# Performance work log

Measured on AMD Instinct MI355X. Metric: run time of the kernel, lower is better.

## Reference

```python
import jax, jax.numpy as jnp
import numpy as np

B, S, D_MODEL = 1, 1024, 1024
D_CKV, D_CQ = 256, 512
N_HEAD, D_HEAD, D_ROPE = 8, 64, 32


def setup_inputs() -> dict:
    key = jax.random.key(0)
    ks = jax.random.split(key, 12)
    def w(k, shape):
        return jax.random.normal(k, shape, dtype=jnp.float32) * 0.02
    return {
        "x": jax.random.normal(ks[0], (B, S, D_MODEL), dtype=jnp.float32),
        "w_q_idx": w(ks[1], (D_MODEL, N_HEAD * D_HEAD)),
        "w_k_idx": w(ks[2], (D_MODEL, D_HEAD)),
        "w_idx": jnp.ones((N_HEAD,), dtype=jnp.float32),
        "raw_delta": jnp.zeros((D_ROPE // 2,), dtype=jnp.float32),
        "w_dkv": w(ks[3], (D_MODEL, D_CKV)),
        "w_uk": w(ks[4], (D_CKV, N_HEAD * D_HEAD)),
        "w_uv": w(ks[5], (D_CKV, N_HEAD * D_HEAD)),
        "w_dq": w(ks[6], (D_MODEL, D_CQ)),
        "w_uq": w(ks[7], (D_CQ, N_HEAD * D_HEAD)),
        "w_qr": w(ks[8], (D_CQ, N_HEAD * D_ROPE)),
        "w_kr": w(ks[9], (D_MODEL, D_ROPE)),
        "w_out": w(ks[10], (N_HEAD * D_HEAD, D_MODEL)),
        "k_ts": 128,
        "local_window": 64,
    }


def _pope(x, raw_delta, theta):
    # x: (b, L, H, d_rope); positions run along axis 1 (matches torch PoPE)
    delta = -2.0 * jnp.pi * jax.nn.sigmoid(raw_delta)            # (d2,)
    pos = jnp.arange(x.shape[1], dtype=x.dtype)
    ang = pos[None, :, None, None] * theta + delta               # (1, L, 1, d2)
    c, s = jnp.cos(ang), jnp.sin(ang)
    mu1, mu2 = jnp.split(jax.nn.softplus(x), 2, axis=-1)
    return jnp.concatenate((mu1 * c - mu2 * s, mu1 * s + mu2 * c), axis=-1)


def reference(x, w_q_idx, w_k_idx, w_idx, raw_delta, w_dkv, w_uk, w_uv,
              w_dq, w_uq, w_qr, w_kr, w_out, k_ts, local_window):
    b, s, _ = x.shape
    h, dh, dr = N_HEAD, D_HEAD, D_ROPE
    theta = 1.0 / (10000.0 ** (2.0 * jnp.arange(dr // 2, dtype=jnp.float32) / dr))

    # ---- LightningIndexer: per-head relu'd relevance, combined with learned head weights
    qI = (x @ w_q_idx).reshape(b, s, h, dh)
    kI = x @ w_k_idx                                             # (b, s, dh)
    sc = jax.nn.relu(jnp.einsum('bthd,bsd->bths', qI, kI))
    I = jnp.einsum('bths,h->bts', sc, w_idx)

    # ---- TokenSelector: force local window in, mask future out, top-k indices
    qp = jnp.arange(s)[:, None]
    kp = jnp.arange(s)[None, :]
    local = (kp >= qp - local_window + 1) & (kp <= qp)
    causal = kp > qp
    I = jnp.where(local, jnp.inf, I)
    I = jnp.where(causal, -jnp.inf, I)
    k = min(k_ts, s)
    _, idx = jax.lax.top_k(I, k)                                 # (b, s, k) int32

    gather = jax.vmap(lambda t, i: t[i])                         # (s,d),(l,k)->(l,k,d)

    # ---- MLA latent KV, gathered per query
    c_kv = x @ w_dkv                                             # (b, s, d_ckv)
    ckv_sel = gather(c_kv, idx)                                  # (b, s, k, d_ckv)
    key_c = (ckv_sel @ w_uk).reshape(b, s, k, h, dh).transpose(0, 3, 1, 2, 4)
    value = (ckv_sel @ w_uv).reshape(b, s, k, h, dh).transpose(0, 3, 1, 2, 4)

    c_q = x @ w_dq
    query_c = (c_q @ w_uq).reshape(b, s, h, dh).transpose(0, 2, 1, 3)
    query_r = _pope((c_q @ w_qr).reshape(b, s, h, dr), raw_delta, theta).transpose(0, 2, 1, 3)

    # key rope: PoPE applied with positions along the k (selected-token) axis,
    # exactly as the torch code's permute(0,2,1,3) does
    x_sel = gather(x, idx)                                       # (b, s, k, d_model)
    kr = _pope((x_sel @ w_kr).transpose(0, 2, 1, 3), raw_delta, theta).transpose(0, 2, 1, 3)
    key_r = jnp.broadcast_to(kr[:, None], (b, h, s, k, dr))

    query = jnp.concatenate((query_c, query_r), axis=-1)         # (b, h, s, dh+dr)
    keyt = jnp.concatenate((key_c, key_r), axis=-1)              # (b, h, s, k, dh+dr)
    scale = (dh + dr) ** -0.5
    scores = jnp.einsum('bhld,bhlkd->bhlk', query, keyt) * scale
    attn = jax.nn.softmax(scores, axis=-1)
    out = jnp.einsum('bhlk,bhlkd->bhld', attn, value)
    out = out.transpose(0, 2, 1, 3).reshape(b, s, h * dh)
    return out @ w_out
```

## Files before the change

### kernel.cpp

```cpp
#include <hip/hip_runtime.h>
#include <math.h>

#define S_LEN 1024
#define NH 8

typedef __attribute__((ext_vector_type(8))) short bf16x8;
typedef __attribute__((ext_vector_type(4))) float f32x4;

__device__ __forceinline__ float sp_softplus(float x) {
    return fmaxf(x, 0.f) + log1pf(expf(-fabsf(x)));
}

__device__ __forceinline__ unsigned short bfu(float f) {
    unsigned u = __float_as_uint(f);
    unsigned r = (u + 0x7FFFu + ((u >> 16) & 1u)) >> 16;
    return (unsigned short)r;
}

struct FRONT {
    const float *x, *wqidx, *wkidx, *raw_delta, *wuk;
    const float *wdkv, *wdq, *wkr, *wuq, *wqr, *wuv, *wout;
    float *qIP, *kIP, *csc, *css;
    unsigned short *wdkvT, *wdqT, *wkrT, *wuqT, *wqrT, *wuvT, *woutT, *wukb;
};

__global__ __launch_bounds__(256) void front_kernel(FRONT f)
{
    __shared__ float As[2][16][18];
    __shared__ float Bs[2][16][68];
    __shared__ unsigned short tile[64][65];
    int bx = blockIdx.x;
    if (bx < 1152) {
        int gx = bx % 18, gy = bx / 18;
        int half = threadIdx.x >> 7;
        int t = threadIdx.x & 127;
        int u = gx * 2 + half;
        const float* B; float* C;
        int ldb, N, n0, kb;
        if (u < 32) {
            B = f.wqidx; ldb = 512; N = 512;
            C = f.qIP + (long)(u >> 3) * 524288;
            n0 = (u & 7) * 64;
            kb = (u >> 3) * 256;
        } else {
            B = f.wkidx; ldb = 64; N = 64;
            C = f.kIP + (long)(u - 32) * 65536;
            n0 = 0;
            kb = (u - 32) * 256;
        }
        int ke = kb + 256;
        int m0 = gy * 16;
        int ar = t >> 2, ak = t & 3;
        int bk = t >> 3, bn = t & 7;
        int ty = t >> 4, tx = t & 15;

        float4 aN = make_float4(0.f, 0.f, 0.f, 0.f);
        if (t < 64) aN = *(const float4*)(f.x + (long)(m0 + ar) * 1024 + kb + ak * 4);
        float4 b0 = *(const float4*)(B + (long)(kb + bk) * ldb + n0 + bn * 4);
        float4 b1 = *(const float4*)(B + (long)(kb + bk) * ldb + n0 + (bn + 8) * 4);
        float acc[2][4] = {};
        for (int k0 = kb; k0 < ke; k0 += 16) {
            if (t < 64) {
                As[half][ak * 4 + 0][ar] = aN.x;
                As[half][ak * 4 + 1][ar] = aN.y;
                As[half][ak * 4 + 2][ar] = aN.z;
                As[half][ak * 4 + 3][ar] = aN.w;
            }
            *(float4*)&Bs[half][bk][bn * 4] = b0;
            *(float4*)&Bs[half][bk][(bn + 8) * 4] = b1;
            __syncthreads();
            if (k0 + 16 < ke) {
                if (t < 64) aN = *(const float4*)(f.x + (long)(m0 + ar) * 1024 + (k0 + 16) + ak * 4);
                b0 = *(const float4*)(B + (long)(k0 + 16 + bk) * ldb + n0 + bn * 4);
                b1 = *(const float4*)(B + (long)(k0 + 16 + bk) * ldb + n0 + (bn + 8) * 4);
            }
            #pragma unroll
            for (int kk = 0; kk < 16; ++kk) {
                float2 a = *(float2*)&As[half][kk][ty * 2];
                float4 b = *(float4*)&Bs[half][kk][tx * 4];
                acc[0][0] += a.x * b.x; acc[0][1] += a.x * b.y;
                acc[0][2] += a.x * b.z; acc[0][3] += a.x * b.w;
                acc[1][0] += a.y * b.x; acc[1][1] += a.y * b.y;
                acc[1][2] += a.y * b.z; acc[1][3] += a.y * b.w;
            }
            __syncthreads();
        }
        #pragma unroll
        for (int i = 0; i < 2; ++i) {
            float4 v = make_float4(acc[i][0], acc[i][1], acc[i][2], acc[i][3]);
            *(float4*)(C + (long)(m0 + ty * 2 + i) * N + n0 + tx * 4) = v;
        }
    } else if (bx < 1616) {
        int b = bx - 1152;
        const float* srcs[7] = {f.wdkv, f.wdq, f.wkr, f.wuq, f.wqr, f.wuv, f.wout};
        unsigned short* dsts[7] = {f.wdkvT, f.wdqT, f.wkrT, f.wuqT, f.wqrT, f.wuvT, f.woutT};
        const int Ns[7]   = {256, 512, 32, 512, 256, 512, 1024};
        const int Klds[7] = {1024, 1024, 1024, 512, 512, 256, 512};
        const int Ntl[7]  = {4, 8, 1, 8, 4, 8, 16};
        const int bst[8]  = {0, 64, 192, 208, 272, 304, 336, 464};
        int e = 0;
        #pragma unroll
        for (int i = 1; i < 7; ++i) if (b >= bst[i]) e = i;
        int lb = b - bst[e];
        int nt = lb % Ntl[e], kt = lb / Ntl[e];
        const float* src = srcs[e];
        unsigned short* dst = dsts[e];
        int N = Ns[e], Kld = Klds[e];
        int k0 = kt * 64, n0 = nt * 64;
        int t = threadIdx.x;
        int c = t & 63, r4 = t >> 6;
        #pragma unroll
        for (int it = 0; it < 16; ++it) {
            int r = it * 4 + r4;
            float v = (n0 + c < N) ? src[(long)(k0 + r) * N + n0 + c] : 0.f;
            tile[r][c] = bfu(v);
        }
        __syncthreads();
        int wq = t & 7;
        #pragma unroll
        for (int itw = 0; itw < 2; ++itw) {
            int wr = itw * 32 + (t >> 3);
            if (n0 + wr < N) {
                unsigned short v[8];
                #pragma unroll
                for (int j = 0; j < 8; ++j) v[j] = tile[wq * 8 + j][wr];
                *(uint4*)(dst + (long)(n0 + wr) * Kld + k0 + wq * 8) = *(uint4*)v;
            }
        }
    } else if (bx < 1624) {
        int idx = (bx - 1616) * 256 + threadIdx.x;
        int j = idx >> 4, i = idx & 15;
        float rd = f.raw_delta[i];
        float delta = -6.283185307179586f * (1.f / (1.f + expf(-rd)));
        float th = exp2f(-(float)i * 0.83048202372184f);
        float ang = (float)j * th + delta;
        float sv, cv;
        sincosf(ang, &sv, &cv);
        f.csc[idx] = cv;
        f.css[idx] = sv;
    } else {
        int idx = (bx - 1624) * 256 + threadIdx.x;
        f.wukb[idx] = bfu(f.wuk[idx]);
    }
}

struct MFG {
    const float* A[10]; const unsigned short* B[10]; float* C[10];
    int lda[10], ldb[10], ldc[10], K[10], N[10], obf[10];
    int tstart[11]; int ne;
};

__global__ __launch_bounds__(256) void mgemm(MFG mg)
{
    int bx = blockIdx.x, e = 0;
    #pragma unroll
    for (int i = 1; i < 10; ++i) if (i < mg.ne && bx >= mg.tstart[i]) e = i;
    const float* A = mg.A[e];
    const unsigned short* B = mg.B[e];
    float* C = mg.C[e];
    int lda = mg.lda[e], ldb = mg.ldb[e], ldc = mg.ldc[e];
    int K = mg.K[e], N = mg.N[e];
    int m0 = blockIdx.y * 64, n0 = (bx - mg.tstart[e]) * 64;

    __shared__ unsigned short As[64][40];
    __shared__ unsigned short Bs[64][40];
    int t = threadIdx.x;
    int srow = t >> 2, skq = t & 3;
    int wid = t >> 6, l = t & 63;
    int wm = (wid >> 1) * 32, wn = (wid & 1) * 32;
    int fr = l & 15, fk = (l >> 4) * 8;
    bool bok = (n0 + srow) < N;

    f32x4 acc00 = {0.f, 0.f, 0.f, 0.f};
    f32x4 acc01 = {0.f, 0.f, 0.f, 0.f};
    f32x4 acc10 = {0.f, 0.f, 0.f, 0.f};
    f32x4 acc11 = {0.f, 0.f, 0.f, 0.f};

    for (int k0 = 0; k0 < K; k0 += 32) {
        {
            const float* ap = A + (long)(m0 + srow) * lda + k0 + skq * 8;
            float4 v0 = *(const float4*)ap;
            float4 v1 = *(const float4*)(ap + 4);
            unsigned short* d = &As[srow][skq * 8];
            d[0] = bfu(v0.x); d[1] = bfu(v0.y); d[2] = bfu(v0.z); d[3] = bfu(v0.w);
            d[4] = bfu(v1.x); d[5] = bfu(v1.y); d[6] = bfu(v1.z); d[7] = bfu(v1.w);
        }
        {
            uint4 bv = make_uint4(0u, 0u, 0u, 0u);
            if (bok) bv = *(const uint4*)(B + (long)(n0 + srow) * ldb + k0 + skq * 8);
            *(uint4*)&Bs[srow][skq * 8] = bv;
        }
        __syncthreads();
        bf16x8 a0 = *(bf16x8*)&As[wm + fr][fk];
        bf16x8 a1 = *(bf16x8*)&As[wm + 16 + fr][fk];
        bf16x8 b0 = *(bf16x8*)&Bs[wn + fr][fk];
        bf16x8 b1 = *(bf16x8*)&Bs[wn + 16 + fr][fk];
        acc00 = __builtin_amdgcn_mfma_f32_16x16x32_bf16(a0, b0, acc00, 0, 0, 0);
        acc01 = __builtin_amdgcn_mfma_f32_16x16x32_bf16(a0, b1, acc01, 0, 0, 0);
        acc10 = __builtin_amdgcn_mfma_f32_16x16x32_bf16(a1, b0, acc10, 0, 0, 0);
        acc11 = __builtin_amdgcn_mfma_f32_16x16x32_bf16(a1, b1, acc11, 0, 0, 0);
        __syncthreads();
    }
    int crow = (l >> 4) * 4;
    int col0 = n0 + wn + fr, col1 = n0 + wn + 16 + fr;
    if (mg.obf[e]) {
        unsigned short* Cu = (unsigned short*)C;
        if (col0 < N) {
            #pragma unroll
            for (int r = 0; r < 4; ++r) {
                Cu[(long)(m0 + wm + crow + r) * ldc + col0]      = bfu(acc00[r]);
                Cu[(long)(m0 + wm + 16 + crow + r) * ldc + col0] = bfu(acc10[r]);
            }
        }
        if (col1 < N) {
            #pragma unroll
            for (int r = 0; r < 4; ++r) {
                Cu[(long)(m0 + wm + crow + r) * ldc + col1]      = bfu(acc01[r]);
                Cu[(long)(m0 + wm + 16 + crow + r) * ldc + col1] = bfu(acc11[r]);
            }
        }
    } else {
        if (col0 < N) {
            #pragma unroll
            for (int r = 0; r < 4; ++r) {
                C[(long)(m0 + wm + crow + r) * ldc + col0]      = acc00[r];
                C[(long)(m0 + wm + 16 + crow + r) * ldc + col0] = acc10[r];
            }
        }
        if (col1 < N) {
            #pragma unroll
            for (int r = 0; r < 4; ++r) {
                C[(long)(m0 + wm + crow + r) * ldc + col1]      = acc01[r];
                C[(long)(m0 + wm + 16 + crow + r) * ldc + col1] = acc11[r];
            }
        }
    }
}

struct MIDARG {
    const float *qIP, *kIP, *w_idx; float* I;
    const float* qc; const unsigned short* wukb; float* qabs;
    const float *qrp, *raw_delta; float* qrr;
    const float* xkr; float* mu;
};

__global__ __launch_bounds__(256) void mid_kernel(MIDARG g)
{
    __shared__ __align__(16) char smem[26112];
    int b = blockIdx.x;
    int t = threadIdx.x;
    if (b < 512) {
        int sb = b % 16, tb = b / 16;
        if (sb * 64 > tb * 32 + 31) return;
        int t0 = tb * 32, s0 = sb * 64;
        float (*ksT)[68] = (float(*)[68])smem;
        float (*qs)[68]  = (float(*)[68])(smem + 17408);
        {
            int r = t & 63, q = t >> 6;
            #pragma unroll
            for (int u = 0; u < 4; ++u) {
                int c4 = q * 4 + u;
                long off = (long)(s0 + r) * 64 + c4 * 4;
                float4 v = *(const float4*)(g.kIP + off);
                #pragma unroll
                for (int s = 1; s < 4; ++s) {
                    float4 v2 = *(const float4*)(g.kIP + (long)s * 65536 + off);
                    v.x += v2.x; v.y += v2.y; v.z += v2.z; v.w += v2.w;
                }
                ksT[c4 * 4 + 0][r] = v.x;
                ksT[c4 * 4 + 1][r] = v.y;
                ksT[c4 * 4 + 2][r] = v.z;
                ksT[c4 * 4 + 3][r] = v.w;
            }
        }
        int ty = t >> 4, tx = t & 15;
        float accI[2][4] = {};
        for (int h = 0; h < 8; ++h) {
            __syncthreads();
            {
                int r = t >> 3, q = t & 7;
                long base = (long)(t0 + r) * 512 + h * 64;
                #pragma unroll
                for (int half = 0; half < 2; ++half) {
                    long off = base + (q + half * 8) * 4;
                    float4 a = *(const float4*)(g.qIP + off);
                    #pragma unroll
                    for (int s = 1; s < 4; ++s) {
                        float4 a1 = *(const float4*)(g.qIP + (long)s * 524288 + off);
                        a.x += a1.x; a.y += a1.y; a.z += a1.z; a.w += a1.w;
                    }
                    *(float4*)&qs[r][(q + half * 8) * 4] = a;
                }
            }
            __syncthreads();
            float acc[2][4] = {};
            #pragma unroll
            for (int dc = 0; dc < 4; ++dc) {
                float a0[16], a1[16];
                #pragma unroll
                for (int u = 0; u < 4; ++u) {
                    float4 v0 = *(float4*)&qs[ty * 2][dc * 16 + u * 4];
                    float4 v1 = *(float4*)&qs[ty * 2 + 1][dc * 16 + u * 4];
                    a0[u * 4 + 0] = v0.x; a0[u * 4 + 1] = v0.y; a0[u * 4 + 2] = v0.z; a0[u * 4 + 3] = v0.w;
                    a1[u * 4 + 0] = v1.x; a1[u * 4 + 1] = v1.y; a1[u * 4 + 2] = v1.z; a1[u * 4 + 3] = v1.w;
                }
                #pragma unroll
                for (int kk = 0; kk < 16; ++kk) {
                    int d = dc * 16 + kk;
                    float4 bb = *(float4*)&ksT[d][tx * 4];
                    acc[0][0] += a0[kk] * bb.x; acc[0][1] += a0[kk] * bb.y;
                    acc[0][2] += a0[kk] * bb.z; acc[0][3] += a0[kk] * bb.w;
                    acc[1][0] += a1[kk] * bb.x; acc[1][1] += a1[kk] * bb.y;
                    acc[1][2] += a1[kk] * bb.z; acc[1][3] += a1[kk] * bb.w;
                }
            }
            float wh = g.w_idx[h];
            #pragma unroll
            for (int i = 0; i < 2; ++i)
                #pragma unroll
                for (int j = 0; j < 4; ++j)
                    accI[i][j] += wh * fmaxf(acc[i][j], 0.f);
        }
        #pragma unroll
        for (int i = 0; i < 2; ++i) {
            float4 v = make_float4(accI[i][0], accI[i][1], accI[i][2], accI[i][3]);
            *(float4*)&g.I[(long)(t0 + ty * 2 + i) * 1024 + s0 + tx * 4] = v;
        }
    } else if (b < 1024) {
        int lb = b - 512;
        int h = lb >> 6, rem = lb & 63;
        int n0 = (rem >> 4) * 64, m0 = (rem & 15) * 64;
        const float* A = g.qc + h * 64;
        const unsigned short* B = g.wukb + h * 64;
        float* C = g.qabs + h * 256;
        unsigned short (*As)[40] = (unsigned short(*)[40])smem;
        unsigned short (*Bs)[40] = (unsigned short(*)[40])(smem + 5120);
        int srow = t >> 2, skq = t & 3;
        int wid = t >> 6, l = t & 63;
        int wm = (wid >> 1) * 32, wn = (wid & 1) * 32;
        int fr = l & 15, fk = (l >> 4) * 8;
        f32x4 acc00 = {0.f, 0.f, 0.f, 0.f};
        f32x4 acc01 = {0.f, 0.f, 0.f, 0.f};
        f32x4 acc10 = {0.f, 0.f, 0.f, 0.f};
        f32x4 acc11 = {0.f, 0.f, 0.f, 0.f};
        for (int k0 = 0; k0 < 64; k0 += 32) {
            {
                const float* ap = A + (long)(m0 + srow) * 512 + k0 + skq * 8;
                float4 v0 = *(const float4*)ap;
                float4 v1 = *(const float4*)(ap + 4);
                unsigned short* d = &As[srow][skq * 8];
                d[0] = bfu(v0.x); d[1] = bfu(v0.y); d[2] = bfu(v0.z); d[3] = bfu(v0.w);
                d[4] = bfu(v1.x); d[5] = bfu(v1.y); d[6] = bfu(v1.z); d[7] = bfu(v1.w);
            }
            {
                uint4 bv = *(const uint4*)(B + (long)(n0 + srow) * 512 + k0 + skq * 8);
                *(uint4*)&Bs[srow][skq * 8] = bv;
            }
            __syncthreads();
            bf16x8 a0 = *(bf16x8*)&As[wm + fr][fk];
            bf16x8 a1 = *(bf16x8*)&As[wm + 16 + fr][fk];
            bf16x8 b0 = *(bf16x8*)&Bs[wn + fr][fk];
            bf16x8 b1 = *(bf16x8*)&Bs[wn + 16 + fr][fk];
            acc00 = __builtin_amdgcn_mfma_f32_16x16x32_bf16(a0, b0, acc00, 0, 0, 0);
            acc01 = __builtin_amdgcn_mfma_f32_16x16x32_bf16(a0, b1, acc01, 0, 0, 0);
            acc10 = __builtin_amdgcn_mfma_f32_16x16x32_bf16(a1, b0, acc10, 0, 0, 0);
            acc11 = __builtin_amdgcn_mfma_f32_16x16x32_bf16(a1, b1, acc11, 0, 0, 0);
            __syncthreads();
        }
        int crow = (l >> 4) * 4;
        int col0 = n0 + wn + fr, col1 = n0 + wn + 16 + fr;
        #pragma unroll
        for (int r = 0; r < 4; ++r) {
            C[(long)(m0 + wm + crow + r) * 2048 + col0]      = acc00[r];
            C[(long)(m0 + wm + 16 + crow + r) * 2048 + col0] = acc10[r];
            C[(long)(m0 + wm + crow + r) * 2048 + col1]      = acc01[r];
            C[(long)(m0 + wm + 16 + crow + r) * 2048 + col1] = acc11[r];
        }
    } else if (b < 1536) {
        int tq = (b - 1024) * 2 + (t >> 7);
        int tt = t & 127;
        int h = tt >> 4, i = tt & 15;
        float rd = g.raw_delta[i];
        float delta = -6.283185307179586f * (1.f / (1.f + expf(-rd)));
        float th = exp2f(-(float)i * 0.83048202372184f);
        float ang = (float)tq * th + delta;
        float sv, cv;
        sincosf(ang, &sv, &cv);
        float m1 = sp_softplus(g.qrp[tq * 256 + h * 32 + i]);
        float m2 = sp_softplus(g.qrp[tq * 256 + h * 32 + 16 + i]);
        g.qrr[tq * 256 + h * 32 + i]      = m1 * cv - m2 * sv;
        g.qrr[tq * 256 + h * 32 + 16 + i] = m1 * sv + m2 * cv;
    } else {
        int i = (b - 1536) * 256 + t;
        g.mu[i] = sp_softplus(g.xkr[i]);
    }
}

__global__ __launch_bounds__(256) void topk_kernel(
    const float* __restrict__ I, int* __restrict__ idxout)
{
    int t = blockIdx.x * 4 + (threadIdx.x >> 6);
    int lane = threadIdx.x & 63;
    int smin = max(0, t - 63);
    int w = min(64, t + 1);
    if (lane < w) idxout[t * 128 + lane] = smin + lane;
    for (int q = t + 1 + lane; q < 128; q += 64)
        idxout[t * 128 + q] = q;
    int f = max(0, t - 63);
    int m = min(f, 64);
    if (m == 0) return;
    const float* row = I + (long)t * 1024;

    unsigned long long key[16];
    #pragma unroll
    for (int g4 = 0; g4 < 4; ++g4) {
        float4 v = *(const float4*)(row + lane * 16 + g4 * 4);
        float vv[4] = {v.x, v.y, v.z, v.w};
        #pragma unroll
        for (int j = 0; j < 4; ++j) {
            int s = lane * 16 + g4 * 4 + j;
            unsigned long long k = 0ull;
            if (s < f) {
                unsigned u = __float_as_uint(vv[j]);
                unsigned ou = (u & 0x80000000u) ? ~u : (u | 0x80000000u);
                k = ((unsigned long long)ou << 32) | (0xFFFFFFFFu - (unsigned)s);
            }
            key[g4 * 4 + j] = k;
        }
    }

    #pragma unroll
    for (int km = 1; km <= 10; ++km) {
        #pragma unroll
        for (int jm = km - 1; jm >= 0; --jm) {
            if (jm >= 4) {
                int lmask = 1 << (jm - 4);
                #pragma unroll
                for (int r = 0; r < 16; ++r) {
                    unsigned long long other = __shfl_xor(key[r], lmask, 64);
                    int i = lane * 16 + r;
                    bool keep_max = (((i & (1 << km)) == 0) == ((i & (1 << jm)) == 0));
                    unsigned long long mx = key[r] > other ? key[r] : other;
                    unsigned long long mn = key[r] > other ? other : key[r];
                    key[r] = keep_max ? mx : mn;
                }
            } else {
                int rmask = 1 << jm;
                #pragma unroll
                for (int r = 0; r < 16; ++r) {
                    if ((r & rmask) == 0) {
                        int r2 = r | rmask;
                        int i = lane * 16 + r;
                        bool keep_max_low = ((i & (1 << km)) == 0);
                        unsigned long long a = key[r], b = key[r2];
                        unsigned long long mx = a > b ? a : b;
                        unsigned long long mn = a > b ? b : a;
                        key[r]  = keep_max_low ? mx : mn;
                        key[r2] = keep_max_low ? mn : mx;
                    }
                }
            }
        }
    }

    if (lane < 4) {
        #pragma unroll
        for (int r = 0; r < 16; ++r) {
            int e = lane * 16 + r;
            if (e < m) {
                int s = (int)(0xFFFFFFFFu - (unsigned)(key[r] & 0xFFFFFFFFull));
                idxout[t * 128 + w + e] = s;
            }
        }
    }
}

__global__ __launch_bounds__(256) void attn_kernel(
    const float* __restrict__ qabs, const float* __restrict__ qrr,
    const unsigned short* __restrict__ ckvb, const float* __restrict__ mu,
    const float* __restrict__ csc, const float* __restrict__ css,
    const int* __restrict__ idxb, float* __restrict__ olat)
{
    __shared__ float sc[8][68];
    __shared__ float hs[16];
    __shared__ int idx_s[128];

    int t = blockIdx.x, tid = threadIdx.x;
    int w = tid >> 6, l = tid & 63;
    const float scale = 0.10206207261596575f;

    if (tid < 128) idx_s[tid] = idxb[t * 128 + tid];

    int hrow = l & 15;
    int kslice = (l >> 4) * 8;
    int hpv = l >> 3;
    int c8 = w * 64 + (l & 7) * 8;

    float mrun0 = -INFINITY, mrun1 = -INFINITY;
    float lrun0 = 0.f, lrun1 = 0.f;
    float acc0 = 0, acc1 = 0, acc2 = 0, acc3 = 0;
    float acc4 = 0, acc5 = 0, acc6 = 0, acc7 = 0;

    __syncthreads();

    #pragma unroll
    for (int chunk = 0; chunk < 2; ++chunk) {
        if (chunk) __syncthreads();

        int r = w * 16 + hrow;
        int src = idx_s[chunk * 64 + r];
        int jglob = chunk * 64 + r;
        f32x4 st = {0.f, 0.f, 0.f, 0.f};
        #pragma unroll 1
        for (int ks = 0; ks < 8; ++ks) {
            bf16x8 af = *(const bf16x8*)(ckvb + (long)src * 256 + ks * 32 + kslice);
            bf16x8 qf = {0, 0, 0, 0, 0, 0, 0, 0};
            if (hrow < 8) {
                const float* qp = qabs + (long)t * 2048 + hrow * 256 + ks * 32 + kslice;
                float4 a = *(const float4*)qp;
                float4 b = *(const float4*)(qp + 4);
                unsigned short qq[8];
                qq[0] = bfu(a.x * scale); qq[1] = bfu(a.y * scale);
                qq[2] = bfu(a.z * scale); qq[3] = bfu(a.w * scale);
                qq[4] = bfu(b.x * scale); qq[5] = bfu(b.y * scale);
                qq[6] = bfu(b.z * scale); qq[7] = bfu(b.w * scale);
                qf = *(bf16x8*)qq;
            }
            st = __builtin_amdgcn_mfma_f32_16x16x32_bf16(af, qf, st, 0, 0, 0);
        }
        {
            int i15 = kslice & 15;
            bool lo = kslice < 16;
            float4 m1a = *(const float4*)(mu + src * 32 + i15);
            float4 m1b = *(const float4*)(mu + src * 32 + i15 + 4);
            float4 m2a = *(const float4*)(mu + src * 32 + 16 + i15);
            float4 m2b = *(const float4*)(mu + src * 32 + 16 + i15 + 4);
            float4 ca = *(const float4*)(csc + jglob * 16 + i15);
            float4 cb = *(const float4*)(csc + jglob * 16 + i15 + 4);
            float4 sa = *(const float4*)(css + jglob * 16 + i15);
            float4 sb = *(const float4*)(css + jglob * 16 + i15 + 4);
            unsigned short hh[8];
            hh[0] = bfu(lo ? m1a.x * ca.x - m2a.x * sa.x : m1a.x * sa.x + m2a.x * ca.x);
            hh[1] = bfu(lo ? m1a.y * ca.y - m2a.y * sa.y : m1a.y * sa.y + m2a.y * ca.y);
            hh[2] = bfu(lo ? m1a.z * ca.z - m2a.z * sa.z : m1a.z * sa.z + m2a.z * ca.z);
            hh[3] = bfu(lo ? m1a.w * ca.w - m2a.w * sa.w : m1a.w * sa.w + m2a.w * ca.w);
            hh[4] = bfu(lo ? m1b.x * cb.x - m2b.x * sb.x : m1b.x * sb.x + m2b.x * cb.x);
            hh[5] = bfu(lo ? m1b.y * cb.y - m2b.y * sb.y : m1b.y * sb.y + m2b.y * cb.y);
            hh[6] = bfu(lo ? m1b.z * cb.z - m2b.z * sb.z : m1b.z * sb.z + m2b.z * cb.z);
            hh[7] = bfu(lo ? m1b.w * cb.w - m2b.w * sb.w : m1b.w * sb.w + m2b.w * cb.w);
            bf16x8 af = *(bf16x8*)hh;
            bf16x8 qf = {0, 0, 0, 0, 0, 0, 0, 0};
            if (hrow < 8) {
                const float* qp = qrr + (long)t * 256 + hrow * 32 + kslice;
                float4 a = *(const float4*)qp;
                float4 b = *(const float4*)(qp + 4);
                unsigned short qq[8];
                qq[0] = bfu(a.x * scale); qq[1] = bfu(a.y * scale);
                qq[2] = bfu(a.z * scale); qq[3] = bfu(a.w * scale);
                qq[4] = bfu(b.x * scale); qq[5] = bfu(b.y * scale);
                qq[6] = bfu(b.z * scale); qq[7] = bfu(b.w * scale);
                qf = *(bf16x8*)qq;
            }
            st = __builtin_amdgcn_mfma_f32_16x16x32_bf16(af, qf, st, 0, 0, 0);
        }
        {
            int srow2 = w * 16 + (l >> 4) * 4;
            if (hrow < 8) {
                #pragma unroll
                for (int rr = 0; rr < 4; ++rr) sc[hrow][srow2 + rr] = st[rr];
            }
        }
        __syncthreads();

        float rh0, rh1;
        {
            int h = 2 * w;
            float v = sc[h][l];
            float mx = v;
            #pragma unroll
            for (int off = 32; off > 0; off >>= 1) mx = fmaxf(mx, __shfl_xor(mx, off));
            float mnew = fmaxf(mrun0, mx);
            float p = expf(v - mnew);
            float ps = p;
            #pragma unroll
            for (int off = 32; off > 0; off >>= 1) ps += __shfl_xor(ps, off);
            rh0 = expf(mrun0 - mnew);
            lrun0 = lrun0 * rh0 + ps;
            mrun0 = mnew;
            sc[h][l] = p;
        }
        {
            int h = 2 * w + 1;
            float v = sc[h][l];
            float mx = v;
            #pragma unroll
            for (int off = 32; off > 0; off >>= 1) mx = fmaxf(mx, __shfl_xor(mx, off));
            float mnew = fmaxf(mrun1, mx);
            float p = expf(v - mnew);
            float ps = p;
            #pragma unroll
            for (int off = 32; off > 0; off >>= 1) ps += __shfl_xor(ps, off);
            rh1 = expf(mrun1 - mnew);
            lrun1 = lrun1 * rh1 + ps;
            mrun1 = mnew;
            sc[h][l] = p;
        }
        if (l == 0) {
            hs[2 * w] = rh0;
            hs[2 * w + 1] = rh1;
            if (chunk == 1) {
                hs[8 + 2 * w] = lrun0;
                hs[8 + 2 * w + 1] = lrun1;
            }
        }
        __syncthreads();

        float rsel = hs[hpv];
        acc0 *= rsel; acc1 *= rsel; acc2 *= rsel; acc3 *= rsel;
        acc4 *= rsel; acc5 *= rsel; acc6 *= rsel; acc7 *= rsel;
        #pragma unroll 4
        for (int j = 0; j < 64; ++j) {
            float p = sc[hpv][j];
            int srcj = idx_s[chunk * 64 + j];
            uint4 vv = *(const uint4*)(ckvb + (long)srcj * 256 + c8);
            acc0 += p * __uint_as_float(vv.x << 16);
            acc1 += p * __uint_as_float(vv.x & 0xffff0000u);
            acc2 += p * __uint_as_float(vv.y << 16);
            acc3 += p * __uint_as_float(vv.y & 0xffff0000u);
            acc4 += p * __uint_as_float(vv.z << 16);
            acc5 += p * __uint_as_float(vv.z & 0xffff0000u);
            acc6 += p * __uint_as_float(vv.w << 16);
            acc7 += p * __uint_as_float(vv.w & 0xffff0000u);
        }
    }

    float inv = 1.f / hs[8 + hpv];
    float* op = olat + (long)t * 2048 + hpv * 256 + c8;
    *(float4*)op       = make_float4(acc0 * inv, acc1 * inv, acc2 * inv, acc3 * inv);
    *(float4*)(op + 4) = make_float4(acc4 * inv, acc5 * inv, acc6 * inv, acc7 * inv);
}

extern "C" void kernel_launch(void* const* d_in, const int* in_sizes, int n_in,
                              void* d_out, int out_size, void* d_ws, size_t ws_size,
                              hipStream_t stream)
{
    const float* x         = (const float*)d_in[0];
    const float* w_q_idx   = (const float*)d_in[1];
    const float* w_k_idx   = (const float*)d_in[2];
    const float* w_idx     = (const float*)d_in[3];
    const float* raw_delta = (const float*)d_in[4];
    const float* w_dkv     = (const float*)d_in[5];
    const float* w_uk      = (const float*)d_in[6];
    const float* w_uv      = (const float*)d_in[7];
    const float* w_dq      = (const float*)d_in[8];
    const float* w_uq      = (const float*)d_in[9];
    const float* w_qr      = (const float*)d_in[10];
    const float* w_kr      = (const float*)d_in[11];
    const float* w_out     = (const float*)d_in[12];
    (void)in_sizes; (void)n_in; (void)out_size; (void)ws_size;
    float* out = (float*)d_out;

    float* ws = (float*)d_ws;
    unsigned short* ckvb = (unsigned short*)ws;   ws += 131072;
    float* cq    = ws;        ws += 1024 * 512;
    float* xkr   = ws;        ws += 1024 * 32;
    float* qrp   = ws;        ws += 1024 * 256;
    float* qrr   = ws;        ws += 1024 * 256;
    float* qc    = ws;        ws += 1024 * 512;
    float* qabs  = ws;        ws += 1024 * 2048;
    float* Ibuf  = ws;        ws += 1024 * 1024;
    int*   idxb  = (int*)ws;  ws += 1024 * 128;
    float* olat  = ws;        ws += 1024 * 2048;
    float* outh  = ws;        ws += 1024 * 512;
    float* mu    = ws;        ws += 1024 * 32;
    float* cscb  = ws;        ws += 128 * 16;
    float* cssb  = ws;        ws += 128 * 16;
    unsigned short* wdkvT = (unsigned short*)ws;  ws += 131072;
    unsigned short* wdqT  = (unsigned short*)ws;  ws += 262144;
    unsigned short* wkrT  = (unsigned short*)ws;  ws += 16384;
    unsigned short* wuqT  = (unsigned short*)ws;  ws += 131072;
    unsigned short* wqrT  = (unsigned short*)ws;  ws += 65536;
    unsigned short* wuvT  = (unsigned short*)ws;  ws += 65536;
    unsigned short* woutT = (unsigned short*)ws;  ws += 262144;
    unsigned short* wukb  = (unsigned short*)ws;  ws += 65536;
    float* part  = ws;        ws += 2359296;
    float* qIP = part;
    float* kIP = part + 2097152;

    {
        FRONT f{};
        f.x = x; f.wqidx = w_q_idx; f.wkidx = w_k_idx; f.raw_delta = raw_delta; f.wuk = w_uk;
        f.wdkv = w_dkv; f.wdq = w_dq; f.wkr = w_kr; f.wuq = w_uq; f.wqr = w_qr;
        f.wuv = w_uv; f.wout = w_out;
        f.qIP = qIP; f.kIP = kIP; f.csc = cscb; f.css = cssb;
        f.wdkvT = wdkvT; f.wdqT = wdqT; f.wkrT = wkrT; f.wuqT = wuqT;
        f.wqrT = wqrT; f.wuvT = wuvT; f.woutT = woutT; f.wukb = wukb;
        front_kernel<<<dim3(2136), dim3(256), 0, stream>>>(f);
    }

    {
        MFG m{};
        for (int i = 0; i < 3; ++i) { m.A[i]=x; m.lda[i]=1024; m.K[i]=1024; }
        m.B[0]=wdkvT; m.C[0]=(float*)ckvb; m.ldb[0]=1024; m.ldc[0]=256; m.N[0]=256; m.obf[0]=1;
        m.B[1]=wdqT;  m.C[1]=cq;           m.ldb[1]=1024; m.ldc[1]=512; m.N[1]=512;
        m.B[2]=wkrT;  m.C[2]=xkr;          m.ldb[2]=1024; m.ldc[2]=32;  m.N[2]=32;
        m.tstart[0]=0; m.tstart[1]=4; m.tstart[2]=12; m.tstart[3]=13;
        m.ne = 3;
        mgemm<<<dim3(13, 16), dim3(256), 0, stream>>>(m);
    }

    {
        MFG m{};
        for (int i = 0; i < 2; ++i) { m.A[i]=cq; m.lda[i]=512; m.K[i]=512; }
        m.B[0]=wuqT; m.C[0]=qc;  m.ldb[0]=512; m.ldc[0]=512; m.N[0]=512;
        m.B[1]=wqrT; m.C[1]=qrp; m.ldb[1]=512; m.ldc[1]=256; m.N[1]=256;
        m.tstart[0]=0; m.tstart[1]=8; m.tstart[2]=12;
        m.ne = 2;
        mgemm<<<dim3(12, 16), dim3(256), 0, stream>>>(m);
    }

    {
        MIDARG g{};
        g.qIP = qIP; g.kIP = kIP; g.w_idx = w_idx; g.I = Ibuf;
        g.qc = qc; g.wukb = wukb; g.qabs = qabs;
        g.qrp = qrp; g.raw_delta = raw_delta; g.qrr = qrr;
        g.xkr = xkr; g.mu = mu;
        mid_kernel<<<dim3(1664), dim3(256), 0, stream>>>(g);
    }

    topk_kernel<<<dim3(256), dim3(256), 0, stream>>>(Ibuf, idxb);

    attn_kernel<<<dim3(1024), dim3(256), 0, stream>>>(qabs, qrr, ckvb, mu, cscb, cssb, idxb, olat);

    {
        MFG m{};
        for (int h = 0; h < 8; ++h) {
            m.A[h] = olat + h * 256;      m.lda[h] = 2048; m.K[h] = 256;
            m.B[h] = wuvT + h * 64 * 256; m.ldb[h] = 256;
            m.C[h] = outh + h * 64;       m.ldc[h] = 512;  m.N[h] = 64;
            m.tstart[h] = h;
        }
        m.tstart[8] = 8;
        m.ne = 8;
        mgemm<<<dim3(8, 16), dim3(256), 0, stream>>>(m);
    }

    {
        MFG m{};
        m.A[0] = outh;  m.lda[0] = 512; m.K[0] = 512;
        m.B[0] = woutT; m.ldb[0] = 512;
        m.C[0] = out;   m.ldc[0] = 1024; m.N[0] = 1024;
        m.tstart[0] = 0; m.tstart[1] = 16;
        m.ne = 1;
        mgemm<<<dim3(16, 16), dim3(256), 0, stream>>>(m);
    }
}
```

Measured before the change: 193.8 us.

## Co-schedule indexer and top-k with independent projection GEMMs in shared launches

The work is regrouped into stages by data dependence. The indexer score computation now runs inside the same launch as the first down-projection GEMMs, and top-k selection runs alongside the second-stage up-projection GEMMs. What remains of the old mid kernel becomes a smaller kernel, which removes one launch and lets independent work fill idle CUs. In exchange, the s1 blocks reserve the larger shared-memory allocation even for GEMM tiles, which may reduce occupancy.

Result: faster. 163.8 us (median of 2 runs) (-15.5%).

```diff
diff --git a/kernel.cpp b/kernel.cpp
--- a/kernel.cpp
+++ b/kernel.cpp
@@ -144,26 +144,12 @@
     }
 }
 
-struct MFG {
-    const float* A[10]; const unsigned short* B[10]; float* C[10];
-    int lda[10], ldb[10], ldc[10], K[10], N[10], obf[10];
-    int tstart[11]; int ne;
-};
-
-__global__ __launch_bounds__(256) void mgemm(MFG mg)
-{
-    int bx = blockIdx.x, e = 0;
-    #pragma unroll
-    for (int i = 1; i < 10; ++i) if (i < mg.ne && bx >= mg.tstart[i]) e = i;
-    const float* A = mg.A[e];
-    const unsigned short* B = mg.B[e];
-    float* C = mg.C[e];
-    int lda = mg.lda[e], ldb = mg.ldb[e], ldc = mg.ldc[e];
-    int K = mg.K[e], N = mg.N[e];
-    int m0 = blockIdx.y * 64, n0 = (bx - mg.tstart[e]) * 64;
-
-    __shared__ unsigned short As[64][40];
-    __shared__ unsigned short Bs[64][40];
+__device__ __forceinline__ void mgemm_body(
+    const float* A, const unsigned short* B, float* C,
+    int lda, int ldb, int ldc, int K, int N, int obf, int m0, int n0, char* smem)
+{
+    unsigned short (*As)[40] = (unsigned short(*)[40])smem;
+    unsigned short (*Bs)[40] = (unsigned short(*)[40])(smem + 5120);
     int t = threadIdx.x;
     int srow = t >> 2, skq = t & 3;
     int wid = t >> 6, l = t & 63;
@@ -203,7 +189,7 @@
     }
     int crow = (l >> 4) * 4;
     int col0 = n0 + wn + fr, col1 = n0 + wn + 16 + fr;
-    if (mg.obf[e]) {
+    if (obf) {
         unsigned short* Cu = (unsigned short*)C;
         if (col0 < N) {
             #pragma unroll
@@ -237,169 +223,93 @@
     }
 }
 
-struct MIDARG {
-    const float *qIP, *kIP, *w_idx; float* I;
-    const float* qc; const unsigned short* wukb; float* qabs;
-    const float *qrp, *raw_delta; float* qrr;
-    const float* xkr; float* mu;
-};
-
-__global__ __launch_bounds__(256) void mid_kernel(MIDARG g)
-{
-    __shared__ __align__(16) char smem[26112];
-    int b = blockIdx.x;
+__device__ __forceinline__ void indexer_body(
+    const float* qIP, const float* kIP, const float* w_idx, float* I,
+    int b, char* smem)
+{
+    int sb = b % 16, tb = b / 16;
+    if (sb * 64 > tb * 32 + 31) return;
+    int t0 = tb * 32, s0 = sb * 64;
+    float (*ksT)[68] = (float(*)[68])smem;
+    float (*qs)[68]  = (float(*)[68])(smem + 17408);
     int t = threadIdx.x;
-    if (b < 512) {
-        int sb = b % 16, tb = b / 16;
-        if (sb * 64 > tb * 32 + 31) return;
-        int t0 = tb * 32, s0 = sb * 64;
-        float (*ksT)[68] = (float(*)[68])smem;
-        float (*qs)[68]  = (float(*)[68])(smem + 17408);
+    {
+        int r = t & 63, q = t >> 6;
+        #pragma unroll
+        for (int u = 0; u < 4; ++u) {
+            int c4 = q * 4 + u;
+            long off = (long)(s0 + r) * 64 + c4 * 4;
+            float4 v = *(const float4*)(kIP + off);
+            #pragma unroll
+            for (int s = 1; s < 4; ++s) {
+                float4 v2 = *(const float4*)(kIP + (long)s * 65536 + off);
+                v.x += v2.x; v.y += v2.y; v.z += v2.z; v.w += v2.w;
+            }
+            ksT[c4 * 4 + 0][r] = v.x;
+            ksT[c4 * 4 + 1][r] = v.y;
+            ksT[c4 * 4 + 2][r] = v.z;
+            ksT[c4 * 4 + 3][r] = v.w;
+        }
+    }
+    int ty = t >> 4, tx = t & 15;
+    float accI[2][4] = {};
+    for (int h = 0; h < 8; ++h) {
+        __syncthreads();
         {
-            int r = t & 63, q = t >> 6;
-            #pragma unroll
-            for (int u = 0; u < 4; ++u) {
-                int c4 = q * 4 + u;
-                long off = (long)(s0 + r) * 64 + c4 * 4;
-                float4 v = *(const float4*)(g.kIP + off);
+            int r = t >> 3, q = t & 7;
+            long base = (long)(t0 + r) * 512 + h * 64;
+            #pragma unroll
+            for (int half = 0; half < 2; ++half) {
+                long off = base + (q + half * 8) * 4;
+                float4 a = *(const float4*)(qIP + off);
                 #pragma unroll
                 for (int s = 1; s < 4; ++s) {
-                    float4 v2 = *(const float4*)(g.kIP + (long)s * 65536 + off);
-                    v.x += v2.x; v.y += v2.y; v.z += v2.z; v.w += v2.w;
+                    float4 a1 = *(const float4*)(qIP + (long)s * 524288 + off);
+                    a.x += a1.x; a.y += a1.y; a.z += a1.z; a.w += a1.w;
                 }
-                ksT[c4 * 4 + 0][r] = v.x;
-                ksT[c4 * 4 + 1][r] = v.y;
-                ksT[c4 * 4 + 2][r] = v.z;
-                ksT[c4 * 4 + 3][r] = v.w;
-            }
-        }
-        int ty = t >> 4, tx = t & 15;
-        float accI[2][4] = {};
-        for (int h = 0; h < 8; ++h) {
-            __syncthreads();
-            {
-                int r = t >> 3, q = t & 7;
-                long base = (long)(t0 + r) * 512 + h * 64;
-                #pragma unroll
-                for (int half = 0; half < 2; ++half) {
-                    long off = base + (q + half * 8) * 4;
-                    float4 a = *(const float4*)(g.qIP + off);
-                    #pragma unroll
-                    for (int s = 1; s < 4; ++s) {
-                        float4 a1 = *(const float4*)(g.qIP + (long)s * 524288 + off);
-                        a.x += a1.x; a.y += a1.y; a.z += a1.z; a.w += a1.w;
-                    }
-                    *(float4*)&qs[r][(q + half * 8) * 4] = a;
-                }
-            }
-            __syncthreads();
-            float acc[2][4] = {};
-            #pragma unroll
-            for (int dc = 0; dc < 4; ++dc) {
-                float a0[16], a1[16];
-                #pragma unroll
-                for (int u = 0; u < 4; ++u) {
-                    float4 v0 = *(float4*)&qs[ty * 2][dc * 16 + u * 4];
-                    float4 v1 = *(float4*)&qs[ty * 2 + 1][dc * 16 + u * 4];
-                    a0[u * 4 + 0] = v0.x; a0[u * 4 + 1] = v0.y; a0[u * 4 + 2] = v0.z; a0[u * 4 + 3] = v0.w;
-                    a1[u * 4 + 0] = v1.x; a1[u * 4 + 1] = v1.y; a1[u * 4 + 2] = v1.z; a1[u * 4 + 3] = v1.w;
-                }
-                #pragma unroll
-                for (int kk = 0; kk < 16; ++kk) {
-                    int d = dc * 16 + kk;
-                    float4 bb = *(float4*)&ksT[d][tx * 4];
-                    acc[0][0] += a0[kk] * bb.x; acc[0][1] += a0[kk] * bb.y;
-                    acc[0][2] += a0[kk] * bb.z; acc[0][3] += a0[kk] * bb.w;
-                    acc[1][0] += a1[kk] * bb.x; acc[1][1] += a1[kk] * bb.y;
-                    acc[1][2] += a1[kk] * bb.z; acc[1][3] += a1[kk] * bb.w;
-                }
-            }
-            float wh = g.w_idx[h];
-            #pragma unroll
-            for (int i = 0; i < 2; ++i)
-                #pragma unroll
-                for (int j = 0; j < 4; ++j)
-                    accI[i][j] += wh * fmaxf(acc[i][j], 0.f);
-        }
-        #pragma unroll
-        for (int i = 0; i < 2; ++i) {
-            float4 v = make_float4(accI[i][0], accI[i][1], accI[i][2], accI[i][3]);
-            *(float4*)&g.I[(long)(t0 + ty * 2 + i) * 1024 + s0 + tx * 4] = v;
-        }
-    } else if (b < 1024) {
-        int lb = b - 512;
-        int h = lb >> 6, rem = lb & 63;
-        int n0 = (rem >> 4) * 64, m0 = (rem & 15) * 64;
-        const float* A = g.qc + h * 64;
-        const unsigned short* B = g.wukb + h * 64;
-        float* C = g.qabs + h * 256;
-        unsigned short (*As)[40] = (unsigned short(*)[40])smem;
-        unsigned short (*Bs)[40] = (unsigned short(*)[40])(smem + 5120);
-        int srow = t >> 2, skq = t & 3;
-        int wid = t >> 6, l = t & 63;
-        int wm = (wid >> 1) * 32, wn = (wid & 1) * 32;
-        int fr = l & 15, fk = (l >> 4) * 8;
-        f32x4 acc00 = {0.f, 0.f, 0.f, 0.f};
-        f32x4 acc01 = {0.f, 0.f, 0.f, 0.f};
-        f32x4 acc10 = {0.f, 0.f, 0.f, 0.f};
-        f32x4 acc11 = {0.f, 0.f, 0.f, 0.f};
-        for (int k0 = 0; k0 < 64; k0 += 32) {
-            {
-                const float* ap = A + (long)(m0 + srow) * 512 + k0 + skq * 8;
-                float4 v0 = *(const float4*)ap;
-                float4 v1 = *(const float4*)(ap + 4);
-                unsigned short* d = &As[srow][skq * 8];
-                d[0] = bfu(v0.x); d[1] = bfu(v0.y); d[2] = bfu(v0.z); d[3] = bfu(v0.w);
-                d[4] = bfu(v1.x); d[5] = bfu(v1.y); d[6] = bfu(v1.z); d[7] = bfu(v1.w);
-            }
-            {
-                uint4 bv = *(const uint4*)(B + (long)(n0 + srow) * 512 + k0 + skq * 8);
-                *(uint4*)&Bs[srow][skq * 8] = bv;
-            }
-            __syncthreads();
-            bf16x8 a0 = *(bf16x8*)&As[wm + fr][fk];
-            bf16x8 a1 = *(bf16x8*)&As[wm + 16 + fr][fk];
-            bf16x8 b0 = *(bf16x8*)&Bs[wn + fr][fk];
-            bf16x8 b1 = *(bf16x8*)&Bs[wn + 16 + fr][fk];
-            acc00 = __builtin_amdgcn_mfma_f32_16x16x32_bf16(a0, b0, acc00, 0, 0, 0);
-            acc01 = __builtin_amdgcn_mfma_f32_16x16x32_bf16(a0, b1, acc01, 0, 0, 0);
-            acc10 = __builtin_amdgcn_mfma_f32_16x16x32_bf16(a1, b0, acc10, 0, 0, 0);
-            acc11 = __builtin_amdgcn_mfma_f32_16x16x32_bf16(a1, b1, acc11, 0, 0, 0);
-            __syncthreads();
-        }
-        int crow = (l >> 4) * 4;
-        int col0 = n0 + wn + fr, col1 = n0 + wn + 16 + fr;
-        #pragma unroll
-        for (int r = 0; r < 4; ++r) {
-            C[(long)(m0 + wm + crow + r) * 2048 + col0]      = acc00[r];
-            C[(long)(m0 + wm + 16 + crow + r) * 2048 + col0] = acc10[r];
-            C[(long)(m0 + wm + crow + r) * 2048 + col1]      = acc01[r];
-            C[(long)(m0 + wm + 16 + crow + r) * 2048 + col1] = acc11[r];
-        }
-    } else if (b < 1536) {
-        int tq = (b - 1024) * 2 + (t >> 7);
-        int tt = t & 127;
-        int h = tt >> 4, i = tt & 15;
-        float rd = g.raw_delta[i];
-        float delta = -6.283185307179586f * (1.f / (1.f + expf(-rd)));
-        float th = exp2f(-(float)i * 0.83048202372184f);
-        float ang = (float)tq * th + delta;
-        float sv, cv;
-        sincosf(ang, &sv, &cv);
-        float m1 = sp_softplus(g.qrp[tq * 256 + h * 32 + i]);
-        float m2 = sp_softplus(g.qrp[tq * 256 + h * 32 + 16 + i]);
-        g.qrr[tq * 256 + h * 32 + i]      = m1 * cv - m2 * sv;
-        g.qrr[tq * 256 + h * 32 + 16 + i] = m1 * sv + m2 * cv;
-    } else {
-        int i = (b - 1536) * 256 + t;
-        g.mu[i] = sp_softplus(g.xkr[i]);
-    }
-}
-
-__global__ __launch_bounds__(256) void topk_kernel(
-    const float* __restrict__ I, int* __restrict__ idxout)
-{
-    int t = blockIdx.x * 4 + (threadIdx.x >> 6);
+                *(float4*)&qs[r][(q + half * 8) * 4] = a;
+            }
+        }
+        __syncthreads();
+        float acc[2][4] = {};
+        #pragma unroll
+        for (int dc = 0; dc < 4; ++dc) {
+            float a0[16], a1[16];
+            #pragma unroll
+            for (int u = 0; u < 4; ++u) {
+                float4 v0 = *(float4*)&qs[ty * 2][dc * 16 + u * 4];
+                float4 v1 = *(float4*)&qs[ty * 2 + 1][dc * 16 + u * 4];
+                a0[u * 4 + 0] = v0.x; a0[u * 4 + 1] = v0.y; a0[u * 4 + 2] = v0.z; a0[u * 4 + 3] = v0.w;
+                a1[u * 4 + 0] = v1.x; a1[u * 4 + 1] = v1.y; a1[u * 4 + 2] = v1.z; a1[u * 4 + 3] = v1.w;
+            }
+            #pragma unroll
+            for (int kk = 0; kk < 16; ++kk) {
+                int d = dc * 16 + kk;
+                float4 bb = *(float4*)&ksT[d][tx * 4];
+                acc[0][0] += a0[kk] * bb.x; acc[0][1] += a0[kk] * bb.y;
+                acc[0][2] += a0[kk] * bb.z; acc[0][3] += a0[kk] * bb.w;
+                acc[1][0] += a1[kk] * bb.x; acc[1][1] += a1[kk] * bb.y;
+                acc[1][2] += a1[kk] * bb.z; acc[1][3] += a1[kk] * bb.w;
+            }
+        }
+        float wh = w_idx[h];
+        #pragma unroll
+        for (int i = 0; i < 2; ++i)
+            #pragma unroll
+            for (int j = 0; j < 4; ++j)
+                accI[i][j] += wh * fmaxf(acc[i][j], 0.f);
+    }
+    #pragma unroll
+    for (int i = 0; i < 2; ++i) {
+        float4 v = make_float4(accI[i][0], accI[i][1], accI[i][2], accI[i][3]);
+        *(float4*)&I[(long)(t0 + ty * 2 + i) * 1024 + s0 + tx * 4] = v;
+    }
+}
+
+__device__ __forceinline__ void topk_body(
+    const float* I, int* idxout, int b)
+{
+    int t = b * 4 + (threadIdx.x >> 6);
     int lane = threadIdx.x & 63;
     int smin = max(0, t - 63);
     int w = min(64, t + 1);
@@ -452,9 +362,9 @@
                         int r2 = r | rmask;
                         int i = lane * 16 + r;
                         bool keep_max_low = ((i & (1 << km)) == 0);
-                        unsigned long long a = key[r], b = key[r2];
-                        unsigned long long mx = a > b ? a : b;
-                        unsigned long long mn = a > b ? b : a;
+                        unsigned long long a = key[r], b2 = key[r2];
+                        unsigned long long mx = a > b2 ? a : b2;
+                        unsigned long long mn = a > b2 ? b2 : a;
                         key[r]  = keep_max_low ? mx : mn;
                         key[r2] = keep_max_low ? mn : mx;
                     }
@@ -473,6 +383,100 @@
             }
         }
     }
+}
+
+struct S1ARG {
+    const float* x;
+    const unsigned short *wdkvT, *wdqT, *wkrT;
+    unsigned short* ckvb; float *cq, *xkr;
+    const float *qIP, *kIP, *w_idx; float* I;
+};
+
+__global__ __launch_bounds__(256) void s1_kernel(S1ARG g)
+{
+    __shared__ __align__(16) char smem[26112];
+    int bx = blockIdx.x;
+    if (bx < 208) {
+        int xi = bx % 13, m0 = (bx / 13) * 64;
+        if (xi < 4)       mgemm_body(g.x, g.wdkvT, (float*)g.ckvb, 1024, 1024, 256, 1024, 256, 1, m0, xi * 64, smem);
+        else if (xi < 12) mgemm_body(g.x, g.wdqT,  g.cq,           1024, 1024, 512, 1024, 512, 0, m0, (xi - 4) * 64, smem);
+        else              mgemm_body(g.x, g.wkrT,  g.xkr,          1024, 1024, 32,  1024, 32,  0, m0, 0, smem);
+    } else {
+        indexer_body(g.qIP, g.kIP, g.w_idx, g.I, bx - 208, smem);
+    }
+}
+
+struct S2ARG {
+    const float* cq;
+    const unsigned short *wuqT, *wqrT;
+    float *qc, *qrp;
+    const float* I; int* idxb;
+};
+
+__global__ __launch_bounds__(256) void s2_kernel(S2ARG g)
+{
+    __shared__ __align__(16) char smem[10240];
+    int bx = blockIdx.x;
+    if (bx < 192) {
+        int xi = bx % 12, m0 = (bx / 12) * 64;
+        if (xi < 8) mgemm_body(g.cq, g.wuqT, g.qc,  512, 512, 512, 512, 512, 0, m0, xi * 64, smem);
+        else        mgemm_body(g.cq, g.wqrT, g.qrp, 512, 512, 256, 512, 256, 0, m0, (xi - 8) * 64, smem);
+    } else {
+        topk_body(g.I, g.idxb, bx - 192);
+    }
+}
+
+struct MID2 {
+    const float* qc; const unsigned short* wukb; float* qabs;
+    const float *qrp, *raw_delta; float* qrr;
+    const float* xkr; float* mu;
+};
+
+__global__ __launch_bounds__(256) void mid2_kernel(MID2 g)
+{
+    __shared__ __align__(16) char smem[10240];
+    int b = blockIdx.x;
+    int t = threadIdx.x;
+    if (b < 512) {
+        int h = b >> 6, rem = b & 63;
+        int n0 = (rem >> 4) * 64, m0 = (rem & 15) * 64;
+        mgemm_body(g.qc + h * 64, g.wukb + h * 64, g.qabs + h * 256,
+                   512, 512, 2048, 64, 256, 0, m0, n0, smem);
+    } else if (b < 1024) {
+        int tq = (b - 512) * 2 + (t >> 7);
+        int tt = t & 127;
+        int h = tt >> 4, i = tt & 15;
+        float rd = g.raw_delta[i];
+        float delta = -6.283185307179586f * (1.f / (1.f + expf(-rd)));
+        float th = exp2f(-(float)i * 0.83048202372184f);
+        float ang = (float)tq * th + delta;
+        float sv, cv;
+        sincosf(ang, &sv, &cv);
+        float m1 = sp_softplus(g.qrp[tq * 256 + h * 32 + i]);
+        float m2 = sp_softplus(g.qrp[tq * 256 + h * 32 + 16 + i]);
+        g.qrr[tq * 256 + h * 32 + i]      = m1 * cv - m2 * sv;
+        g.qrr[tq * 256 + h * 32 + 16 + i] = m1 * sv + m2 * cv;
+    } else {
+        int i = (b - 1024) * 256 + t;
+        g.mu[i] = sp_softplus(g.xkr[i]);
+    }
+}
+
+struct MFG {
+    const float* A[10]; const unsigned short* B[10]; float* C[10];
+    int lda[10], ldb[10], ldc[10], K[10], N[10], obf[10];
+    int tstart[11]; int ne;
+};
+
+__global__ __launch_bounds__(256) void mgemm(MFG mg)
+{
+    __shared__ __align__(16) char smem[10240];
+    int bx = blockIdx.x, e = 0;
+    #pragma unroll
+    for (int i = 1; i < 10; ++i) if (i < mg.ne && bx >= mg.tstart[i]) e = i;
+    mgemm_body(mg.A[e], mg.B[e], mg.C[e], mg.lda[e], mg.ldb[e], mg.ldc[e],
+               mg.K[e], mg.N[e], mg.obf[e], blockIdx.y * 64,
+               (bx - mg.tstart[e]) * 64, smem);
 }
 
 __global__ __launch_bounds__(256) void attn_kernel(
@@ -699,36 +703,28 @@
     }
 
     {
-        MFG m{};
-        for (int i = 0; i < 3; ++i) { m.A[i]=x; m.lda[i]=1024; m.K[i]=1024; }
-        m.B[0]=wdkvT; m.C[0]=(float*)ckvb; m.ldb[0]=1024; m.ldc[0]=256; m.N[0]=256; m.obf[0]=1;
-        m.B[1]=wdqT;  m.C[1]=cq;           m.ldb[1]=1024; m.ldc[1]=512; m.N[1]=512;
-        m.B[2]=wkrT;  m.C[2]=xkr;          m.ldb[2]=1024; m.ldc[2]=32;  m.N[2]=32;
-        m.tstart[0]=0; m.tstart[1]=4; m.tstart[2]=12; m.tstart[3]=13;
-        m.ne = 3;
-        mgemm<<<dim3(13, 16), dim3(256), 0, stream>>>(m);
+        S1ARG g{};
+        g.x = x; g.wdkvT = wdkvT; g.wdqT = wdqT; g.wkrT = wkrT;
+        g.ckvb = ckvb; g.cq = cq; g.xkr = xkr;
+        g.qIP = qIP; g.kIP = kIP; g.w_idx = w_idx; g.I = Ibuf;
+        s1_kernel<<<dim3(720), dim3(256), 0, stream>>>(g);
     }
 
     {
-        MFG m{};
-        for (int i = 0; i < 2; ++i) { m.A[i]=cq; m.lda[i]=512; m.K[i]=512; }
-        m.B[0]=wuqT; m.C[0]=qc;  m.ldb[0]=512; m.ldc[0]=512; m.N[0]=512;
-        m.B[1]=wqrT; m.C[1]=qrp; m.ldb[1]=512; m.ldc[1]=256; m.N[1]=256;
-        m.tstart[0]=0; m.tstart[1]=8; m.tstart[2]=12;
-        m.ne = 2;
-        mgemm<<<dim3(12, 16), dim3(256), 0, stream>>>(m);
+        S2ARG g{};
+        g.cq = cq; g.wuqT = wuqT; g.wqrT = wqrT;
+        g.qc = qc; g.qrp = qrp;
+        g.I = Ibuf; g.idxb = idxb;
+        s2_kernel<<<dim3(448), dim3(256), 0, stream>>>(g);
     }
 
     {
-        MIDARG g{};
-        g.qIP = qIP; g.kIP = kIP; g.w_idx = w_idx; g.I = Ibuf;
+        MID2 g{};
         g.qc = qc; g.wukb = wukb; g.qabs = qabs;
         g.qrp = qrp; g.raw_delta = raw_delta; g.qrr = qrr;
         g.xkr = xkr; g.mu = mu;
-        mid_kernel<<<dim3(1664), dim3(256), 0, stream>>>(g);
-    }
-
-    topk_kernel<<<dim3(256), dim3(256), 0, stream>>>(Ibuf, idxb);
+        mid2_kernel<<<dim3(1152), dim3(256), 0, stream>>>(g);
+    }
 
     attn_kernel<<<dim3(1024), dim3(256), 0, stream>>>(qabs, qrr, ckvb, mu, cscb, cssb, idxb, olat);
 
```
